# Optimization experiments

Measured on AMD Instinct MI355X. Metric: run time of the kernel, lower is better.

## Reference

```python
import jax, jax.numpy as jnp
import numpy as np
import math

D = 2048
N_HEADS = 16
D_HEAD = D // N_HEADS
B = 2
L = 2048


def _rope_tables(seq_len, d_head, base=10000.0):
    # standard half-rotation RoPE tables, shape [L, d_head]
    inv_freq = 1.0 / (base ** (jnp.arange(0, d_head, 2, dtype=jnp.float32) / d_head))
    ang = jnp.arange(seq_len, dtype=jnp.float32)[:, None] * inv_freq[None, :]  # [L, d_head/2]
    cos = jnp.concatenate([jnp.cos(ang), jnp.cos(ang)], axis=-1)  # [L, d_head]
    sin = jnp.concatenate([jnp.sin(ang), jnp.sin(ang)], axis=-1)
    return cos, sin


def _apply_rope(x, cos, sin):
    # x: [B, H, L, d_head]; rotate_half convention
    half = x.shape[-1] // 2
    x_rot = jnp.concatenate([-x[..., half:], x[..., :half]], axis=-1)
    return x * cos[None, None, :, :] + x_rot * sin[None, None, :, :]


def setup_inputs() -> dict:
    key = jax.random.key(0)
    k1, k2, k3 = jax.random.split(key, 3)
    x = jax.random.normal(k1, (B, L, D), dtype=jnp.float32)
    w_qkv = jax.random.normal(k2, (D, 3 * D), dtype=jnp.float32) * (1.0 / math.sqrt(D))
    w_out = jax.random.normal(k3, (D, D), dtype=jnp.float32) * (1.0 / math.sqrt(D))
    s_qk = jnp.asarray(math.sqrt(D_HEAD), dtype=jnp.float32)  # init sqrt(d_head)
    return {"x": x, "w_qkv": w_qkv, "w_out": w_out, "s_qk": s_qk}


def reference(x, w_qkv, w_out, s_qk):
    Bs, Ls, Ds = x.shape
    qkv = jnp.einsum("bld,de->ble", x, w_qkv).reshape(Bs, Ls, 3, N_HEADS, D_HEAD)
    q, k, v = qkv[:, :, 0], qkv[:, :, 1], qkv[:, :, 2]
    # -> [B, H, L, d_head]
    q = jnp.transpose(q, (0, 2, 1, 3))
    k = jnp.transpose(k, (0, 2, 1, 3))
    v = jnp.transpose(v, (0, 2, 1, 3))
    cos, sin = _rope_tables(Ls, D_HEAD)
    q = _apply_rope(q, cos, sin)
    k = _apply_rope(k, cos, sin)
    # L2-normalize per head (torch F.normalize eps=1e-12)
    q = q / jnp.maximum(jnp.linalg.norm(q, axis=-1, keepdims=True), 1e-12)
    k = k / jnp.maximum(jnp.linalg.norm(k, axis=-1, keepdims=True), 1e-12)
    # softmax((q*s_qk) @ k^T) with causal mask, scale=1.0
    scores = jnp.einsum("bhqd,bhkd->bhqk", q * s_qk, k)
    causal = jnp.tril(jnp.ones((Ls, Ls), dtype=bool))
    scores = jnp.where(causal[None, None, :, :], scores, -jnp.inf)
    attn = jax.nn.softmax(scores, axis=-1)
    out = jnp.einsum("bhqk,bhkd->bhqd", attn, v)
    out = jnp.transpose(out, (0, 2, 1, 3)).reshape(Bs, Ls, Ds)
    return jnp.einsum("bld,de->ble", out, w_out)
```

## Files before the change

### kernel.cpp

```cpp
#include <hip/hip_runtime.h>
#include <math.h>


#define D 2048
#define NH 16
#define DH 128
#define BB 2
#define LL 2048
#define BHD (BB*NH)
#define MROWS (BB*LL)
#define KDIM D

typedef __attribute__((ext_vector_type(8))) short short8;
typedef __attribute__((ext_vector_type(4))) float floatx4;

__device__ __forceinline__ unsigned short f2bf(float f) {
    unsigned u = __float_as_uint(f);
    unsigned r = u + 0x7FFFu + ((u >> 16) & 1u);
    return (unsigned short)(r >> 16);
}
__device__ __forceinline__ float bf2f(unsigned short u) {
    return __uint_as_float(((unsigned)u) << 16);
}

__device__ __forceinline__ void async16(const void* g, void* lds) {
    __builtin_amdgcn_global_load_lds(
        (const __attribute__((address_space(1))) unsigned int*)g,
        (__attribute__((address_space(3))) unsigned int*)lds, 16, 0, 0);
}

template<int CTRL>
__device__ __forceinline__ float dpp_movf(float x) {
    return __int_as_float(__builtin_amdgcn_update_dpp(
        0, __float_as_int(x), CTRL, 0xF, 0xF, true));
}
__device__ __forceinline__ float row_max16(float x) {
    x = fmaxf(x, dpp_movf<0xB1>(x));
    x = fmaxf(x, dpp_movf<0x4E>(x));
    x = fmaxf(x, dpp_movf<0x124>(x));
    x = fmaxf(x, dpp_movf<0x128>(x));
    return x;
}
__device__ __forceinline__ float row_sum16(float x) {
    x += dpp_movf<0xB1>(x);
    x += dpp_movf<0x4E>(x);
    x += dpp_movf<0x124>(x);
    x += dpp_movf<0x128>(x);
    return x;
}

__global__ __launch_bounds__(256)
void cast_bf16_kernel_v2(const float* __restrict__ in,
                         unsigned short* __restrict__ out, int n4)
{
    int i = blockIdx.x * 256 + threadIdx.x;
    if (i < n4) {
        float4 v = ((const float4*)in)[i];
        ushort4 o;
        o.x = f2bf(v.x); o.y = f2bf(v.y); o.z = f2bf(v.z); o.w = f2bf(v.w);
        ((ushort4*)out)[i] = o;
    }
}

__global__ __launch_bounds__(256)
void transpose_cast_kernel_v2(const float* __restrict__ W,
                              unsigned short* __restrict__ Wt, int K, int N)
{
    __shared__ float tile[32][33];
    const int tx = threadIdx.x & 31, ty = threadIdx.x >> 5;
    const int n0 = blockIdx.x * 32, k0 = blockIdx.y * 32;
#pragma unroll
    for (int r = 0; r < 4; r++)
        tile[ty + 8 * r][tx] = W[(size_t)(k0 + ty + 8 * r) * N + n0 + tx];
    __syncthreads();
#pragma unroll
    for (int r = 0; r < 4; r++)
        Wt[(size_t)(n0 + ty + 8 * r) * K + k0 + tx] = f2bf(tile[tx][ty + 8 * r]);
}

__global__ __launch_bounds__(256)
void transpose_v_kernel_v2(const unsigned short* __restrict__ Vb,
                           unsigned short* __restrict__ VtG)
{
    __shared__ unsigned short tile[32][34];
    const int tx = threadIdx.x & 31, ty = threadIdx.x >> 5;
    const int l0 = blockIdx.x * 32, d0 = blockIdx.y * 32;
    const int bh = blockIdx.z;
    const unsigned short* src = Vb + (size_t)bh * LL * DH;
    unsigned short* dst = VtG + (size_t)bh * DH * LL;
#pragma unroll
    for (int r = 0; r < 4; r++)
        tile[ty + 8 * r][tx] = src[(size_t)(l0 + ty + 8 * r) * DH + d0 + tx];
    __syncthreads();
#pragma unroll
    for (int r = 0; r < 4; r++)
        dst[(size_t)(d0 + ty + 8 * r) * LL + l0 + tx] = tile[tx][ty + 8 * r];
}

template<int N, int MODE>
__global__ __launch_bounds__(256)
void mfma_gemm_v2(const unsigned short* __restrict__ A,
                  const unsigned short* __restrict__ Bt,
                  float* __restrict__ C, unsigned short* __restrict__ Qo,
                  unsigned short* __restrict__ Ko, unsigned short* __restrict__ Vo)
{
    __shared__ unsigned short As[128 * 32];
    __shared__ unsigned short Bs[128 * 32];
    const int t = threadIdx.x;
    const int w = t >> 6, lane = t & 63;
    const int lrow = lane & 15, quad = lane >> 4;
    const int m0 = blockIdx.y * 128, n0 = blockIdx.x * 128;
    const int wm = (w >> 1) * 64, wn = (w & 1) * 64;

    floatx4 acc[4][4];
#pragma unroll
    for (int i = 0; i < 4; i++)
#pragma unroll
        for (int j = 0; j < 4; j++) acc[i][j] = (floatx4){0.f, 0.f, 0.f, 0.f};

    const int srow = 32 * w + (lane >> 2);
    const int sseg = (lane & 3) * 8;

    for (int k0 = 0; k0 < KDIM; k0 += 32) {
        __syncthreads();
        async16(&A [(size_t)(m0 + srow)      * KDIM + k0 + sseg], &As[(32 * w)      * 32]);
        async16(&A [(size_t)(m0 + srow + 16) * KDIM + k0 + sseg], &As[(32 * w + 16) * 32]);
        async16(&Bt[(size_t)(n0 + srow)      * KDIM + k0 + sseg], &Bs[(32 * w)      * 32]);
        async16(&Bt[(size_t)(n0 + srow + 16) * KDIM + k0 + sseg], &Bs[(32 * w + 16) * 32]);
        __syncthreads();

        short8 a[4], b[4];
#pragma unroll
        for (int i = 0; i < 4; i++)
            a[i] = *(const short8*)&As[(wm + i * 16 + lrow) * 32 + quad * 8];
#pragma unroll
        for (int j = 0; j < 4; j++)
            b[j] = *(const short8*)&Bs[(wn + j * 16 + lrow) * 32 + quad * 8];
#pragma unroll
        for (int i = 0; i < 4; i++)
#pragma unroll
            for (int j = 0; j < 4; j++)
                acc[i][j] = __builtin_amdgcn_mfma_f32_16x16x32_bf16(a[i], b[j], acc[i][j], 0, 0, 0);
    }

    if (MODE == 0) {
#pragma unroll
        for (int i = 0; i < 4; i++)
#pragma unroll
            for (int j = 0; j < 4; j++) {
                int col = n0 + wn + j * 16 + lrow;
#pragma unroll
                for (int r = 0; r < 4; r++) {
                    int m = m0 + wm + i * 16 + quad * 4 + r;
                    C[(size_t)m * N + col] = acc[i][j][r];
                }
            }
    } else {
        const int s = n0 >> 11;
        const int h = (n0 & 2047) >> 7;
        unsigned short* dst = (s == 0) ? Qo : (s == 1) ? Ko : Vo;
#pragma unroll
        for (int i = 0; i < 4; i++)
#pragma unroll
            for (int j = 0; j < 4; j++) {
                int dh = wn + j * 16 + lrow;
#pragma unroll
                for (int r = 0; r < 4; r++) {
                    int m = m0 + wm + i * 16 + quad * 4 + r;
                    int b = m >> 11, l = m & 2047;
                    dst[(((size_t)b * NH + h) * LL + l) * DH + dh] = f2bf(acc[i][j][r]);
                }
            }
    }
}

__global__ __launch_bounds__(128)
void rope_norm_kernel_v2(unsigned short* __restrict__ Q,
                         unsigned short* __restrict__ K,
                         const float* __restrict__ s_qk_ptr)
{
    const int l  = blockIdx.x;
    const int bh = blockIdx.y;
    const int d  = threadIdx.x;
    __shared__ float sh[128];

    const size_t base = ((size_t)bh * LL + l) * DH + d;
    float qv = bf2f(Q[base]);
    float kv = bf2f(K[base]);

    const int i = d & 63;
    float ang = (float)l * expf(-0.14391157f * (float)i);
    float c = cosf(ang), s = sinf(ang);

    sh[d] = qv; __syncthreads();
    float qrot = (d < 64) ? -sh[d + 64] : sh[d - 64];
    float qr = fmaf(qv, c, qrot * s);
    __syncthreads();

    sh[d] = kv; __syncthreads();
    float krot = (d < 64) ? -sh[d + 64] : sh[d - 64];
    float kr = fmaf(kv, c, krot * s);
    __syncthreads();

    sh[d] = qr * qr; __syncthreads();
    for (int st = 64; st > 0; st >>= 1) {
        if (d < st) sh[d] += sh[d + st];
        __syncthreads();
    }
    float qn = sqrtf(sh[0]);
    __syncthreads();

    sh[d] = kr * kr; __syncthreads();
    for (int st = 64; st > 0; st >>= 1) {
        if (d < st) sh[d] += sh[d + st];
        __syncthreads();
    }
    float kn = sqrtf(sh[0]);

    float sqk = s_qk_ptr[0];
    Q[base] = f2bf(qr / fmaxf(qn, 1e-12f) * sqk);
    K[base] = f2bf(kr / fmaxf(kn, 1e-12f));
}

#define ABQ 64
#define ABK 64
__global__ __launch_bounds__(256)
void attn_mfma_kernel_v4(const unsigned short* __restrict__ Q,
                         const unsigned short* __restrict__ K,
                         const unsigned short* __restrict__ Vt,
                         unsigned short* __restrict__ AOb)
{
    __shared__ __align__(16) unsigned short Ks[2][ABK * DH];
    __shared__ __align__(16) unsigned short Vs[2][DH * ABK];
    __shared__ __align__(16) unsigned short Ps[4][16][72];

    const int t = threadIdx.x;
    const int w = t >> 6, lane = t & 63;
    const int lrow = lane & 15, quad = lane >> 4;
    const int bh = blockIdx.y;
    const int qt = gridDim.x - 1 - blockIdx.x;
    const int q0 = qt * ABQ;
    const int qw = q0 + w * 16;

    const unsigned short* Qb = Q  + (size_t)bh * LL * DH;
    const unsigned short* Kb = K  + (size_t)bh * LL * DH;
    const unsigned short* Vg = Vt + (size_t)bh * DH * LL;

    short8 aq[4];
#pragma unroll
    for (int kk = 0; kk < 4; kk++)
        aq[kk] = *(const short8*)&Qb[(size_t)(qw + lrow) * DH + kk * 32 + quad * 8];

    floatx4 oacc[8];
#pragma unroll
    for (int dt = 0; dt < 8; dt++) oacc[dt] = (floatx4){0.f, 0.f, 0.f, 0.f};
    float mrow[4] = {-1e30f, -1e30f, -1e30f, -1e30f};
    float lsum[4] = {0.f, 0.f, 0.f, 0.f};

    auto STAGE = [&](int tile, int buf) {
        const int k0s = tile * ABK;
#pragma unroll
        for (int c = 0; c < 4; c++) {
            int row = 16 * w + 4 * c;
            int r   = row + (lane >> 4);
            int col = (lane & 15) ^ (r & 7);
            async16(&Kb[(size_t)(k0s + r) * DH + col * 8], &Ks[buf][row * DH]);
        }
#pragma unroll
        for (int c = 0; c < 4; c++) {
            int row = 32 * w + 8 * c;
            int r   = row + (lane >> 3);
            int col = (lane & 7) ^ (r & 7);
            async16(&Vg[(size_t)r * LL + k0s + col * 8], &Vs[buf][row * ABK]);
        }
    };

    const int ntiles = qt + 1;
    STAGE(0, 0);
    __syncthreads();

    int cur = 0;
    for (int tile = 0; tile < ntiles; tile++) {
        const int k0 = tile * ABK;
        if (tile + 1 < ntiles) STAGE(tile + 1, cur ^ 1);

        floatx4 sacc[4];
#pragma unroll
        for (int j = 0; j < 4; j++) sacc[j] = (floatx4){0.f, 0.f, 0.f, 0.f};
        __builtin_amdgcn_s_setprio(1);
#pragma unroll
        for (int kk = 0; kk < 4; kk++) {
#pragma unroll
            for (int j = 0; j < 4; j++) {
                int slot = (kk * 4 + quad) ^ (lrow & 7);
                short8 bk = *(const short8*)&Ks[cur][(j * 16 + lrow) * DH + slot * 8];
                sacc[j] = __builtin_amdgcn_mfma_f32_16x16x32_bf16(aq[kk], bk, sacc[j], 0, 0, 0);
            }
        }
        __builtin_amdgcn_s_setprio(0);

        if (k0 + ABK - 1 > qw) {
#pragma unroll
            for (int j = 0; j < 4; j++) {
                int key = k0 + j * 16 + lrow;
#pragma unroll
                for (int r = 0; r < 4; r++) {
                    int q = qw + quad * 4 + r;
                    if (key > q) sacc[j][r] = -1e30f;
                }
            }
        }

        float alpha[4];
#pragma unroll
        for (int r = 0; r < 4; r++) {
            float mt = fmaxf(fmaxf(sacc[0][r], sacc[1][r]),
                             fmaxf(sacc[2][r], sacc[3][r]));
            mt = row_max16(mt);
            float mn = fmaxf(mrow[r], mt);
            alpha[r] = __expf(mrow[r] - mn);
            mrow[r] = mn;
        }
#pragma unroll
        for (int r = 0; r < 4; r++) {
            float rs = 0.f;
#pragma unroll
            for (int j = 0; j < 4; j++) {
                float p = __expf(sacc[j][r] - mrow[r]);
                rs += p;
                Ps[w][quad * 4 + r][j * 16 + lrow] = f2bf(p);
            }
            rs = row_sum16(rs);
            lsum[r] = lsum[r] * alpha[r] + rs;
        }

#pragma unroll
        for (int dt = 0; dt < 8; dt++)
#pragma unroll
            for (int r = 0; r < 4; r++) oacc[dt][r] *= alpha[r];
        __builtin_amdgcn_s_setprio(1);
#pragma unroll
        for (int kk2 = 0; kk2 < 2; kk2++) {
            short8 pa = *(const short8*)&Ps[w][lrow][kk2 * 32 + quad * 8];
#pragma unroll
            for (int dt = 0; dt < 8; dt++) {
                int slot = (kk2 * 4 + quad) ^ (lrow & 7);
                short8 bv = *(const short8*)&Vs[cur][(dt * 16 + lrow) * ABK + slot * 8];
                oacc[dt] = __builtin_amdgcn_mfma_f32_16x16x32_bf16(pa, bv, oacc[dt], 0, 0, 0);
            }
        }
        __builtin_amdgcn_s_setprio(0);

        __syncthreads();
        cur ^= 1;
    }

    const int b = bh >> 4, h = bh & 15;
#pragma unroll
    for (int r = 0; r < 4; r++) {
        float inv = 1.f / lsum[r];
        int q = qw + quad * 4 + r;
        size_t base = ((size_t)b * LL + q) * D + h * DH;
#pragma unroll
        for (int dt = 0; dt < 8; dt++)
            AOb[base + dt * 16 + lrow] = f2bf(oacc[dt][r] * inv);
    }
}

extern "C" void kernel_launch(void* const* d_in, const int* in_sizes, int n_in,
                              void* d_out, int out_size, void* d_ws, size_t ws_size,
                              hipStream_t stream)
{
    const float* x     = (const float*)d_in[0];
    const float* w_qkv = (const float*)d_in[1];
    const float* w_out = (const float*)d_in[2];
    const float* s_qk  = (const float*)d_in[3];
    float* out = (float*)d_out;

    const size_t SZ = (size_t)BB * NH * LL * DH;
    unsigned short* u = (unsigned short*)d_ws;
    unsigned short* xb    = u;
    unsigned short* wqkvT = xb    + (size_t)MROWS * KDIM;
    unsigned short* woutT = wqkvT + (size_t)(3 * D) * KDIM;
    unsigned short* Qb    = woutT + (size_t)D * KDIM;
    unsigned short* Kb    = Qb + SZ;
    unsigned short* Vb    = Kb + SZ;
    unsigned short* VtG   = Vb + SZ;

    cast_bf16_kernel_v2<<<(MROWS * KDIM / 4 + 255) / 256, 256, 0, stream>>>(
        x, xb, MROWS * KDIM / 4);
    transpose_cast_kernel_v2<<<dim3(3 * D / 32, KDIM / 32), 256, 0, stream>>>(
        w_qkv, wqkvT, KDIM, 3 * D);
    mfma_gemm_v2<3 * D, 1><<<dim3(3 * D / 128, MROWS / 128), 256, 0, stream>>>(
        xb, wqkvT, nullptr, Qb, Kb, Vb);
    rope_norm_kernel_v2<<<dim3(LL, BHD), 128, 0, stream>>>(Qb, Kb, s_qk);
    transpose_v_kernel_v2<<<dim3(LL / 32, DH / 32, BHD), 256, 0, stream>>>(Vb, VtG);
    attn_mfma_kernel_v4<<<dim3(LL / ABQ, BHD), 256, 0, stream>>>(Qb, Kb, VtG, xb);
    transpose_cast_kernel_v2<<<dim3(D / 32, D / 32), 256, 0, stream>>>(
        w_out, woutT, D, D);
    mfma_gemm_v2<D, 0><<<dim3(D / 128, MROWS / 128), 256, 0, stream>>>(
        xb, woutT, out, nullptr, nullptr, nullptr);
}
```

Measured before the change: 503.4 us.

## Double attention query tile per block to reuse K/V tiles across two row groups

```diff
diff --git a/kernel.cpp b/kernel.cpp
--- a/kernel.cpp
+++ b/kernel.cpp
@@ -222,40 +222,49 @@
     K[base] = f2bf(kr / fmaxf(kn, 1e-12f));
 }
 
-#define ABQ 64
+#define ABQ 128
 #define ABK 64
-__global__ __launch_bounds__(256)
-void attn_mfma_kernel_v4(const unsigned short* __restrict__ Q,
+__global__ __launch_bounds__(256, 2)
+void attn_mfma_kernel_v5(const unsigned short* __restrict__ Q,
                          const unsigned short* __restrict__ K,
                          const unsigned short* __restrict__ Vt,
                          unsigned short* __restrict__ AOb)
 {
     __shared__ __align__(16) unsigned short Ks[2][ABK * DH];
     __shared__ __align__(16) unsigned short Vs[2][DH * ABK];
-    __shared__ __align__(16) unsigned short Ps[4][16][72];
+    __shared__ __align__(16) unsigned short Ps[4][32][64];
 
     const int t = threadIdx.x;
     const int w = t >> 6, lane = t & 63;
     const int lrow = lane & 15, quad = lane >> 4;
-    const int bh = blockIdx.y;
-    const int qt = gridDim.x - 1 - blockIdx.x;
+    const int bh = blockIdx.x;
+    const int y  = blockIdx.y;
+    const int qt = (y < 8) ? (15 - y) : (y - 8);
     const int q0 = qt * ABQ;
-    const int qw = q0 + w * 16;
+    const int qw = q0 + w * 32;
 
     const unsigned short* Qb = Q  + (size_t)bh * LL * DH;
     const unsigned short* Kb = K  + (size_t)bh * LL * DH;
     const unsigned short* Vg = Vt + (size_t)bh * DH * LL;
 
-    short8 aq[4];
-#pragma unroll
-    for (int kk = 0; kk < 4; kk++)
-        aq[kk] = *(const short8*)&Qb[(size_t)(qw + lrow) * DH + kk * 32 + quad * 8];
-
-    floatx4 oacc[8];
-#pragma unroll
-    for (int dt = 0; dt < 8; dt++) oacc[dt] = (floatx4){0.f, 0.f, 0.f, 0.f};
-    float mrow[4] = {-1e30f, -1e30f, -1e30f, -1e30f};
-    float lsum[4] = {0.f, 0.f, 0.f, 0.f};
+    short8 aq[2][4];
+#pragma unroll
+    for (int h = 0; h < 2; h++)
+#pragma unroll
+        for (int kk = 0; kk < 4; kk++)
+            aq[h][kk] = *(const short8*)&Qb[(size_t)(qw + 16 * h + lrow) * DH
+                                            + kk * 32 + quad * 8];
+
+    floatx4 oacc[2][8];
+#pragma unroll
+    for (int h = 0; h < 2; h++)
+#pragma unroll
+        for (int dt = 0; dt < 8; dt++) oacc[h][dt] = (floatx4){0.f, 0.f, 0.f, 0.f};
+    float mrow[2][4], lsum[2][4];
+#pragma unroll
+    for (int h = 0; h < 2; h++)
+#pragma unroll
+        for (int r = 0; r < 4; r++) { mrow[h][r] = -1e30f; lsum[h][r] = 0.f; }
 
     auto STAGE = [&](int tile, int buf) {
         const int k0s = tile * ABK;
@@ -275,7 +284,7 @@
         }
     };
 
-    const int ntiles = qt + 1;
+    const int ntiles = 2 * qt + 2;
     STAGE(0, 0);
     __syncthreads();
 
@@ -284,9 +293,11 @@
         const int k0 = tile * ABK;
         if (tile + 1 < ntiles) STAGE(tile + 1, cur ^ 1);
 
-        floatx4 sacc[4];
-#pragma unroll
-        for (int j = 0; j < 4; j++) sacc[j] = (floatx4){0.f, 0.f, 0.f, 0.f};
+        floatx4 sacc[2][4];
+#pragma unroll
+        for (int h = 0; h < 2; h++)
+#pragma unroll
+            for (int j = 0; j < 4; j++) sacc[h][j] = (floatx4){0.f, 0.f, 0.f, 0.f};
         __builtin_amdgcn_s_setprio(1);
 #pragma unroll
         for (int kk = 0; kk < 4; kk++) {
@@ -294,59 +305,71 @@
             for (int j = 0; j < 4; j++) {
                 int slot = (kk * 4 + quad) ^ (lrow & 7);
                 short8 bk = *(const short8*)&Ks[cur][(j * 16 + lrow) * DH + slot * 8];
-                sacc[j] = __builtin_amdgcn_mfma_f32_16x16x32_bf16(aq[kk], bk, sacc[j], 0, 0, 0);
+                sacc[0][j] = __builtin_amdgcn_mfma_f32_16x16x32_bf16(aq[0][kk], bk, sacc[0][j], 0, 0, 0);
+                sacc[1][j] = __builtin_amdgcn_mfma_f32_16x16x32_bf16(aq[1][kk], bk, sacc[1][j], 0, 0, 0);
             }
         }
         __builtin_amdgcn_s_setprio(0);
 
-        if (k0 + ABK - 1 > qw) {
-#pragma unroll
-            for (int j = 0; j < 4; j++) {
-                int key = k0 + j * 16 + lrow;
-#pragma unroll
-                for (int r = 0; r < 4; r++) {
-                    int q = qw + quad * 4 + r;
-                    if (key > q) sacc[j][r] = -1e30f;
+#pragma unroll
+        for (int h = 0; h < 2; h++) {
+            if (k0 + ABK - 1 > qw + 16 * h) {
+#pragma unroll
+                for (int j = 0; j < 4; j++) {
+                    int key = k0 + j * 16 + lrow;
+#pragma unroll
+                    for (int r = 0; r < 4; r++) {
+                        int q = qw + 16 * h + quad * 4 + r;
+                        if (key > q) sacc[h][j][r] = -1e30f;
+                    }
                 }
             }
         }
 
-        float alpha[4];
-#pragma unroll
-        for (int r = 0; r < 4; r++) {
-            float mt = fmaxf(fmaxf(sacc[0][r], sacc[1][r]),
-                             fmaxf(sacc[2][r], sacc[3][r]));
-            mt = row_max16(mt);
-            float mn = fmaxf(mrow[r], mt);
-            alpha[r] = __expf(mrow[r] - mn);
-            mrow[r] = mn;
-        }
-#pragma unroll
-        for (int r = 0; r < 4; r++) {
-            float rs = 0.f;
-#pragma unroll
-            for (int j = 0; j < 4; j++) {
-                float p = __expf(sacc[j][r] - mrow[r]);
-                rs += p;
-                Ps[w][quad * 4 + r][j * 16 + lrow] = f2bf(p);
-            }
-            rs = row_sum16(rs);
-            lsum[r] = lsum[r] * alpha[r] + rs;
-        }
-
-#pragma unroll
-        for (int dt = 0; dt < 8; dt++)
-#pragma unroll
-            for (int r = 0; r < 4; r++) oacc[dt][r] *= alpha[r];
+#pragma unroll
+        for (int h = 0; h < 2; h++) {
+            float alpha[4];
+#pragma unroll
+            for (int r = 0; r < 4; r++) {
+                float mt = fmaxf(fmaxf(sacc[h][0][r], sacc[h][1][r]),
+                                 fmaxf(sacc[h][2][r], sacc[h][3][r]));
+                mt = row_max16(mt);
+                float mn = fmaxf(mrow[h][r], mt);
+                alpha[r] = __expf(mrow[h][r] - mn);
+                mrow[h][r] = mn;
+            }
+#pragma unroll
+            for (int r = 0; r < 4; r++) {
+                int rowp = 16 * h + quad * 4 + r;
+                float rs = 0.f;
+#pragma unroll
+                for (int j = 0; j < 4; j++) {
+                    float p = __expf(sacc[h][j][r] - mrow[h][r]);
+                    rs += p;
+                    int slot = (2 * j + (lrow >> 3)) ^ (rowp & 7);
+                    Ps[w][rowp][slot * 8 + (lrow & 7)] = f2bf(p);
+                }
+                rs = row_sum16(rs);
+                lsum[h][r] = lsum[h][r] * alpha[r] + rs;
+            }
+#pragma unroll
+            for (int dt = 0; dt < 8; dt++)
+#pragma unroll
+                for (int r = 0; r < 4; r++) oacc[h][dt][r] *= alpha[r];
+        }
+
         __builtin_amdgcn_s_setprio(1);
 #pragma unroll
         for (int kk2 = 0; kk2 < 2; kk2++) {
-            short8 pa = *(const short8*)&Ps[w][lrow][kk2 * 32 + quad * 8];
+            int pslot = (kk2 * 4 + quad) ^ (lrow & 7);
+            short8 pa0 = *(const short8*)&Ps[w][lrow][pslot * 8];
+            short8 pa1 = *(const short8*)&Ps[w][16 + lrow][pslot * 8];
 #pragma unroll
             for (int dt = 0; dt < 8; dt++) {
                 int slot = (kk2 * 4 + quad) ^ (lrow & 7);
                 short8 bv = *(const short8*)&Vs[cur][(dt * 16 + lrow) * ABK + slot * 8];
-                oacc[dt] = __builtin_amdgcn_mfma_f32_16x16x32_bf16(pa, bv, oacc[dt], 0, 0, 0);
+                oacc[0][dt] = __builtin_amdgcn_mfma_f32_16x16x32_bf16(pa0, bv, oacc[0][dt], 0, 0, 0);
+                oacc[1][dt] = __builtin_amdgcn_mfma_f32_16x16x32_bf16(pa1, bv, oacc[1][dt], 0, 0, 0);
             }
         }
         __builtin_amdgcn_s_setprio(0);
@@ -355,16 +378,18 @@
         cur ^= 1;
     }
 
-    const int b = bh >> 4, h = bh & 15;
-#pragma unroll
-    for (int r = 0; r < 4; r++) {
-        float inv = 1.f / lsum[r];
-        int q = qw + quad * 4 + r;
-        size_t base = ((size_t)b * LL + q) * D + h * DH;
-#pragma unroll
-        for (int dt = 0; dt < 8; dt++)
-            AOb[base + dt * 16 + lrow] = f2bf(oacc[dt][r] * inv);
-    }
+    const int b = bh >> 4, hd = bh & 15;
+#pragma unroll
+    for (int h = 0; h < 2; h++)
+#pragma unroll
+        for (int r = 0; r < 4; r++) {
+            float inv = 1.f / lsum[h][r];
+            int q = qw + 16 * h + quad * 4 + r;
+            size_t base = ((size_t)b * LL + q) * D + hd * DH;
+#pragma unroll
+            for (int dt = 0; dt < 8; dt++)
+                AOb[base + dt * 16 + lrow] = f2bf(oacc[h][dt][r] * inv);
+        }
 }
 
 extern "C" void kernel_launch(void* const* d_in, const int* in_sizes, int n_in,
@@ -395,7 +420,7 @@
         xb, wqkvT, nullptr, Qb, Kb, Vb);
     rope_norm_kernel_v2<<<dim3(LL, BHD), 128, 0, stream>>>(Qb, Kb, s_qk);
     transpose_v_kernel_v2<<<dim3(LL / 32, DH / 32, BHD), 256, 0, stream>>>(Vb, VtG);
-    attn_mfma_kernel_v4<<<dim3(LL / ABQ, BHD), 256, 0, stream>>>(Qb, Kb, VtG, xb);
+    attn_mfma_kernel_v5<<<dim3(BHD, LL / ABQ), 256, 0, stream>>>(Qb, Kb, VtG, xb);
     transpose_cast_kernel_v2<<<dim3(D / 32, D / 32), 256, 0, stream>>>(
         w_out, woutT, D, D);
     mfma_gemm_v2<D, 0><<<dim3(D / 128, MROWS / 128), 256, 0, stream>>>(
```

Result: faster. 438.5 us (-12.9%).
